# Optimization experiments

Measured on AMD Instinct MI355X. Metric: run time of the kernel, lower is better.

## Reference

```python
import jax, jax.numpy as jnp
import numpy as np

H = 128  # rnn_size

def setup_inputs() -> dict:
    key = jax.random.key(0)
    ks = jax.random.split(key, 12)
    B, T, F = 64, 2048, 64
    s = lambda k, shape, fan: jax.random.normal(k, shape, jnp.float32) * (1.0 / np.sqrt(fan))
    return {
        "x":  jax.random.normal(ks[0], (B, T, F), jnp.float32),
        # LSTM params (Keras gate order: i, f, c(g), o)
        "W":  s(ks[1], (F, 4 * H), F),
        "U":  s(ks[2], (H, 4 * H), H),
        "b":  jnp.zeros((4 * H,), jnp.float32),
        # Dense stack
        "W1": s(ks[3], (H, 128), H),   "b1": jnp.zeros((128,), jnp.float32),
        "W2": s(ks[4], (128, 128), 128), "b2": jnp.zeros((128,), jnp.float32),
        "W3": s(ks[5], (128, 32), 128),  "b3": jnp.zeros((32,), jnp.float32),
        "W4": s(ks[6], (32, 1), 32),     "b4": jnp.zeros((1,), jnp.float32),
    }

def _lstm(x, W, U, b):
    # x: [B,T,F] -> outputs h_t for all t: [B,T,H]
    B, T, _ = x.shape
    xp = jnp.einsum('btf,fg->btg', x, W) + b        # precompute input projection [B,T,4H]
    xp = jnp.transpose(xp, (1, 0, 2))               # [T,B,4H] for scan

    def step(carry, xt):
        h, c = carry
        z = xt + h @ U                              # [B,4H]
        i, f, g, o = jnp.split(z, 4, axis=-1)       # Keras gate order i,f,c,o
        i = jax.nn.sigmoid(i)
        f = jax.nn.sigmoid(f)
        g = jnp.tanh(g)
        o = jax.nn.sigmoid(o)
        c = f * c + i * g
        h = o * jnp.tanh(c)
        return (h, c), h

    h0 = jnp.zeros((B, H), x.dtype)
    c0 = jnp.zeros((B, H), x.dtype)
    _, hs = jax.lax.scan(step, (h0, c0), xp)        # hs: [T,B,H]
    return jnp.transpose(hs, (1, 0, 2))             # [B,T,H]

def reference(x, W, U, b, W1, b1, W2, b2, W3, b3, W4, b4):
    h = _lstm(x, W, U, b)                           # [B,T,H]
    h = h @ W1 + b1                                 # d1 (linear)
    h = jax.nn.relu(h @ W2 + b2)                    # d2
    h = jax.nn.relu(h @ W3 + b3)                    # d3
    out = jax.nn.sigmoid(h @ W4 + b4)               # d4 -> [B,T,1]
    return out.reshape(out.shape[0], -1, 1)         # Reshape((-1,1)) is identity here
```

## Files before the change

kernel.cpp:

```cpp
#include <hip/hip_runtime.h>
#include <hip/hip_fp16.h>
#include <cstdint>
#include <cstddef>

typedef _Float16 hh2   __attribute__((ext_vector_type(2)));
typedef _Float16 f16x8 __attribute__((ext_vector_type(8)));
typedef float    f32x4 __attribute__((ext_vector_type(4)));
typedef int      i32x4 __attribute__((ext_vector_type(4)));

__device__ __forceinline__ float fdot2u(unsigned a, unsigned b, float c) {
#if __has_builtin(__builtin_amdgcn_fdot2)
    return __builtin_amdgcn_fdot2(__builtin_bit_cast(hh2, a),
                                  __builtin_bit_cast(hh2, b), c, false);
#else
    float r;
    asm("v_dot2_f32_f16 %0, %1, %2, %3" : "=v"(r) : "v"(a), "v"(b), "v"(c));
    return r;
#endif
}

__device__ __forceinline__ unsigned packh2f(float x, float y) {
    hh2 v; v.x = (_Float16)x; v.y = (_Float16)y;
    return __builtin_bit_cast(unsigned, v);
}

__device__ __forceinline__ float ex2(float x) {
#if __has_builtin(__builtin_amdgcn_exp2f)
    return __builtin_amdgcn_exp2f(x);
#else
    return exp2f(x);
#endif
}
__device__ __forceinline__ float sig2(float x) {
    return __builtin_amdgcn_rcpf(1.f + ex2(x * -1.442695041f));
}
__device__ __forceinline__ float tanh2(float x) {
    return fmaf(2.f, __builtin_amdgcn_rcpf(1.f + ex2(x * -2.885390082f)), -1.f);
}
__device__ __forceinline__ float sigmoidf_fast(float x) {
    return __builtin_amdgcn_rcpf(1.f + __expf(-x));
}
__device__ __forceinline__ float tanhf_fast(float x) {
    float e = __expf(-2.f * fmaxf(x, -30.f));
    return (1.f - e) * __builtin_amdgcn_rcpf(1.f + e);
}

#define BAR_LGKM() asm volatile("s_waitcnt lgkmcnt(0)\n\ts_barrier" ::: "memory")

__global__ __launch_bounds__(512, 2)
void k_xprojT(const float* __restrict__ x, const float* __restrict__ W,
              const float* __restrict__ bias, __half* __restrict__ xpT,
              int B, int T)
{
    __shared__ unsigned short xst[2][16 * 64];

    const int tid = threadIdx.x;
    const int w   = tid >> 6;
    const int l   = tid & 63;
    const int lj  = l & 15;
    const int hi  = l >> 4;
    const int bb  = blockIdx.x >> 2;
    const int q   = blockIdx.x & 3;

    f16x8 Wf[4][2];
    float bc[4];
#pragma unroll
    for (int cg = 0; cg < 4; ++cg) {
        const int col = cg * 128 + w * 16 + lj;
#pragma unroll
        for (int kk = 0; kk < 2; ++kk)
#pragma unroll
            for (int j = 0; j < 8; ++j)
                Wf[cg][kk][j] = (_Float16)W[(size_t)(kk*32 + hi*8 + j) * 512 + col];
        bc[cg] = bias[col];
    }

    const int nch = (T / 4) / 16;
    const size_t rowbase = (size_t)bb * T + (size_t)q * (T / 4);

    const int srow = tid >> 5;
    const int scp  = tid & 31;

    float2 xn = *(const float2*)(x + (rowbase + srow) * 64 + scp * 2);

    for (int ch = 0; ch < nch; ++ch) {
        unsigned pk = packh2f(xn.x, xn.y);
        *(unsigned*)((char*)xst[ch & 1] +
            (((srow * 128 + scp * 4)) ^ ((srow & 7) << 4))) = pk;
        if (ch + 1 < nch)
            xn = *(const float2*)(x + (rowbase + (ch+1)*16 + srow) * 64 + scp * 2);
        BAR_LGKM();

        f16x8 Axf[2];
#pragma unroll
        for (int kk = 0; kk < 2; ++kk)
            Axf[kk] = *(const f16x8*)((char*)xst[ch & 1] +
                ((lj * 128 + kk * 64 + hi * 16) ^ ((lj & 7) << 4)));

        const size_t c8base = (rowbase + (size_t)ch * 16) >> 3;
#pragma unroll
        for (int cg = 0; cg < 4; ++cg) {
            f32x4 C = {bc[cg], bc[cg], bc[cg], bc[cg]};
            C = __builtin_amdgcn_mfma_f32_16x16x32_f16(Axf[0], Wf[cg][0], C, 0, 0, 0);
            C = __builtin_amdgcn_mfma_f32_16x16x32_f16(Axf[1], Wf[cg][1], C, 0, 0, 0);
            const int col = cg * 128 + w * 16 + lj;
            uint2 u;
            u.x = packh2f(C[0], C[1]);
            u.y = packh2f(C[2], C[3]);
            const size_t hidx = ((c8base + (hi >> 1)) * 512 + col) * 8 + (hi & 1) * 4;
            *(uint2*)((unsigned short*)xpT + hidx) = u;
        }
        BAR_LGKM();
    }
}

__global__ __launch_bounds__(512, 2)
void k_lstm7(const float* __restrict__ U, const __half* __restrict__ xpT,
             __half* __restrict__ hs, int T)
{
    __shared__ unsigned char hring[16][128];

    const int tid = threadIdx.x;
    const int w   = tid >> 6;
    const int l   = tid & 63;
    const int lj  = l & 15;
    const int hi  = l >> 4;
    const int bb  = blockIdx.x;

    i32x4 Bq[4][2];
    float dq[4];
#pragma unroll
    for (int g = 0; g < 4; ++g) {
        const int col = g * 128 + w * 16 + lj;
        float m = 0.f;
        for (int k2 = 0; k2 < 128; ++k2)
            m = fmaxf(m, fabsf(U[(size_t)k2 * 512 + col]));
        const float s = (m > 0.f) ? 127.f / m : 0.f;
        dq[g] = m * (1.f / (127.f * 127.f));
#pragma unroll
        for (int kk = 0; kk < 2; ++kk) {
            int wds[4];
#pragma unroll
            for (int d = 0; d < 4; ++d) {
                unsigned word = 0;
#pragma unroll
                for (int b = 0; b < 4; ++b) {
                    int qv = (int)rintf(
                        U[(size_t)(kk*64 + hi*16 + d*4 + b) * 512 + col] * s);
                    word |= (unsigned)(qv & 255) << (8 * b);
                }
                wds[d] = (int)word;
            }
            Bq[g][kk] = (i32x4){wds[0], wds[1], wds[2], wds[3]};
        }
    }

    if (tid < 32) ((unsigned*)hring[15])[tid] = 0u;

    const uint4* __restrict__ xb = (const uint4*)xpT;
    const size_t xrow = (size_t)bb * (T / 8) * 512;
    int colg[4];
#pragma unroll
    for (int g = 0; g < 4; ++g) colg[g] = g * 128 + w * 16 + lj;

    uint4 qA[4], qB[4];
#pragma unroll
    for (int g = 0; g < 4; ++g) {
        qA[g] = xb[xrow + 0 * 512 + colg[g]];
        qB[g] = xb[xrow + 1 * 512 + colg[g]];
    }

    __half* __restrict__ hsb = hs + (size_t)bb * T * 128;
    float cst = 0.f;

    if (((w >> 2) ^ w) & 1) __builtin_amdgcn_s_setprio(1);

    i32x4 Cq[4] = {{0,0,0,0},{0,0,0,0},{0,0,0,0},{0,0,0,0}};

    __syncthreads();

    const int nbody = T / 16;
    for (int k = 0; k < nbody; ++k) {
#pragma unroll
        for (int p = 0; p < 16; ++p) {
            if (p == 8) {
#pragma unroll
                for (int g = 0; g < 4; ++g)
                    qA[g] = xb[xrow + (size_t)(2*k + 2) * 512 + colg[g]];
            }

            const unsigned char* hrow = &hring[(p + 15) & 15][0];
            i32x4 Aq0 = *(const i32x4*)(hrow + hi * 16);
            i32x4 Aq1 = *(const i32x4*)(hrow + 64 + hi * 16);

            Cq[0][0] = 0; Cq[1][0] = 0; Cq[2][0] = 0; Cq[3][0] = 0;
#pragma unroll
            for (int g = 0; g < 4; ++g) {
                Cq[g] = __builtin_amdgcn_mfma_i32_16x16x64_i8(Aq0, Bq[g][0], Cq[g], 0, 0, 0);
                Cq[g] = __builtin_amdgcn_mfma_i32_16x16x64_i8(Aq1, Bq[g][1], Cq[g], 0, 0, 0);
            }

            float zf[4];
#pragma unroll
            for (int g = 0; g < 4; ++g) {
                const uint4 qq = (p < 8) ? qA[g] : qB[g];
                const int wsel = (p & 7) >> 1;
                unsigned uw = (wsel == 0) ? qq.x : (wsel == 1) ? qq.y
                            : (wsel == 2) ? qq.z : qq.w;
                __half2 hh = __builtin_bit_cast(__half2, uw);
                float xpf = __half2float((p & 1) ? __high2half(hh) : __low2half(hh));
                zf[g] = fmaf((float)Cq[g][0], dq[g], xpf);
            }

            float iv = sig2(zf[0]);
            float fv = sig2(zf[1]);
            float gv = tanh2(zf[2]);
            float ov = sig2(zf[3]);
            cst = fmaf(fv, cst, iv * gv);
            float h = ov * tanh2(cst);

            if (l < 16) {
                hsb[(size_t)(k * 16 + p) * 128 + w * 16 + lj] = __float2half(h);
                hring[p][w * 16 + lj] =
                    (unsigned char)(int)rintf(h * 127.f);
            }

            if (p == 15) {
#pragma unroll
                for (int g = 0; g < 4; ++g)
                    qB[g] = xb[xrow + (size_t)(2*k + 3) * 512 + colg[g]];
            }
            BAR_LGKM();
        }
    }
}

__global__ __launch_bounds__(512, 2)
void k_head(const __half* __restrict__ hs,
            const float* __restrict__ W1, const float* __restrict__ b1,
            const float* __restrict__ W2, const float* __restrict__ b2,
            const float* __restrict__ W3, const float* __restrict__ b3,
            const float* __restrict__ W4, const float* __restrict__ b4,
            float* __restrict__ out, int T)
{
    __shared__ unsigned short hstage[16 * 128];
    __shared__ unsigned short d1buf[16 * 128];
    __shared__ unsigned short d2buf[16 * 128];
    __shared__ unsigned short d3buf[16 * 40];

    const int tid = threadIdx.x;
    const int w   = tid >> 6;
    const int l   = tid & 63;
    const int lj  = l & 15;
    const int hi  = l >> 4;
    const int bb  = blockIdx.x >> 5;
    const int ch0 = (blockIdx.x & 31) * 4;

    const int col1 = w * 16 + lj;
    const int col3 = (w & 1) * 16 + lj;

    f16x8 W1f[4], W2f[4], W3f[4];
#pragma unroll
    for (int kk = 0; kk < 4; ++kk)
#pragma unroll
        for (int j = 0; j < 8; ++j) {
            W1f[kk][j] = (_Float16)W1[(size_t)(kk*32 + hi*8 + j) * 128 + col1];
            W2f[kk][j] = (_Float16)W2[(size_t)(kk*32 + hi*8 + j) * 128 + col1];
            W3f[kk][j] = (_Float16)W3[(size_t)(kk*32 + hi*8 + j) * 32 + col3];
        }
    const float b1c = b1[col1];
    const float b2c = b2[col1];
    const float b3c = b3[col3];
    unsigned w4p[16];
#pragma unroll
    for (int k2 = 0; k2 < 16; ++k2)
        w4p[k2] = packh2f(W4[2*k2], W4[2*k2 + 1]);
    const float b4v = b4[0];

    const __half* __restrict__ hsb = hs + (size_t)bb * T * 128;
    const int srow = tid >> 5;
    const int scp  = tid & 31;

    for (int ch = ch0; ch < ch0 + 4; ++ch) {
        const int t0 = ch * 16;
        uint2 hv = *(const uint2*)(hsb + (size_t)(t0 + srow) * 128 + scp * 4);
        *(uint2*)((char*)hstage + ((srow * 256 + scp * 8) ^ ((srow & 7) << 4))) = hv;
        __syncthreads();

        f16x8 A[4];
#pragma unroll
        for (int kk = 0; kk < 4; ++kk)
            A[kk] = *(const f16x8*)((char*)hstage +
                ((lj * 256 + kk * 64 + hi * 16) ^ ((lj & 7) << 4)));
        f32x4 C1 = {b1c, b1c, b1c, b1c};
#pragma unroll
        for (int kk = 0; kk < 4; ++kk)
            C1 = __builtin_amdgcn_mfma_f32_16x16x32_f16(A[kk], W1f[kk], C1, 0, 0, 0);
#pragma unroll
        for (int r = 0; r < 4; ++r) {
            const int row = hi * 4 + r;
            *(unsigned short*)((char*)d1buf + ((row * 256 + col1 * 2) ^ ((row & 7) << 4))) =
                __half_as_ushort(__float2half(C1[r]));
        }
        __syncthreads();

#pragma unroll
        for (int kk = 0; kk < 4; ++kk)
            A[kk] = *(const f16x8*)((char*)d1buf +
                ((lj * 256 + kk * 64 + hi * 16) ^ ((lj & 7) << 4)));
        f32x4 C2 = {b2c, b2c, b2c, b2c};
#pragma unroll
        for (int kk = 0; kk < 4; ++kk)
            C2 = __builtin_amdgcn_mfma_f32_16x16x32_f16(A[kk], W2f[kk], C2, 0, 0, 0);
#pragma unroll
        for (int r = 0; r < 4; ++r) {
            const int row = hi * 4 + r;
            *(unsigned short*)((char*)d2buf + ((row * 256 + col1 * 2) ^ ((row & 7) << 4))) =
                __half_as_ushort(__float2half(fmaxf(C2[r], 0.f)));
        }
        __syncthreads();

#pragma unroll
        for (int kk = 0; kk < 4; ++kk)
            A[kk] = *(const f16x8*)((char*)d2buf +
                ((lj * 256 + kk * 64 + hi * 16) ^ ((lj & 7) << 4)));
        f32x4 C3 = {b3c, b3c, b3c, b3c};
#pragma unroll
        for (int kk = 0; kk < 4; ++kk)
            C3 = __builtin_amdgcn_mfma_f32_16x16x32_f16(A[kk], W3f[kk], C3, 0, 0, 0);
        if (w < 2) {
#pragma unroll
            for (int r = 0; r < 4; ++r) {
                const int row = hi * 4 + r;
                d3buf[row * 40 + col3] =
                    __half_as_ushort(__float2half(fmaxf(C3[r], 0.f)));
            }
        }
        __syncthreads();

        if (w == 0 && l < 16) {
            const unsigned short* dr = &d3buf[l * 40];
            float s0 = b4v, s1 = 0.f;
#pragma unroll
            for (int qq = 0; qq < 4; ++qq) {
                uint4 v = *(const uint4*)(dr + qq * 8);
                s0 = fdot2u(v.x, w4p[qq*4 + 0], s0);
                s1 = fdot2u(v.y, w4p[qq*4 + 1], s1);
                s0 = fdot2u(v.z, w4p[qq*4 + 2], s0);
                s1 = fdot2u(v.w, w4p[qq*4 + 3], s1);
            }
            out[(size_t)bb * T + t0 + l] = sigmoidf_fast(s0 + s1);
        }
        __syncthreads();
    }
}

__global__ __launch_bounds__(512)
void k_lstm_fused(const float* __restrict__ U, const float* __restrict__ x,
                  const float* __restrict__ W, const float* __restrict__ bias,
                  __half* __restrict__ hs, int T)
{
    __shared__ __align__(16) unsigned hbuf[64];
    __shared__ float act[512];
    __shared__ __align__(16) unsigned xrow[32];

    const int g    = threadIdx.x;
    const int bb   = blockIdx.x;
    const int j    = g & 127;
    const int gate = g >> 7;

    unsigned ucol[64];
#pragma unroll
    for (int k2 = 0; k2 < 64; ++k2)
        ucol[k2] = packh2f(U[(2*k2)*512 + g], U[(2*k2+1)*512 + g]);
    unsigned wcol[32];
#pragma unroll
    for (int k2 = 0; k2 < 32; ++k2)
        wcol[k2] = packh2f(W[(2*k2)*512 + g], W[(2*k2+1)*512 + g]);
    const float bg = bias[g];
    const float2* __restrict__ xb2 = (const float2*)(x + (size_t)bb * T * 64);
    if (g < 32) { float2 x0 = xb2[g]; xrow[g] = packh2f(x0.x, x0.y); }
    if (g < 64) hbuf[g] = 0u;
    float c = 0.f;
    __half* __restrict__ hsb = hs + (size_t)bb * T * 128;
    __syncthreads();

    for (int t = 0; t < T; ++t) {
        float2 xn = make_float2(0.f, 0.f);
        if (g < 32 && t + 1 < T) xn = xb2[(size_t)(t + 1) * 32 + g];
        float a0 = bg, a1 = 0.f, a2 = 0.f, a3 = 0.f;
        const uint4* hr = (const uint4*)hbuf;
#pragma unroll
        for (int k8 = 0; k8 < 16; ++k8) {
            uint4 v = hr[k8];
            a0 = fdot2u(v.x, ucol[4*k8+0], a0);
            a1 = fdot2u(v.y, ucol[4*k8+1], a1);
            a2 = fdot2u(v.z, ucol[4*k8+2], a2);
            a3 = fdot2u(v.w, ucol[4*k8+3], a3);
        }
        const uint4* xr = (const uint4*)xrow;
#pragma unroll
        for (int k8 = 0; k8 < 8; ++k8) {
            uint4 v = xr[k8];
            a0 = fdot2u(v.x, wcol[4*k8+0], a0);
            a1 = fdot2u(v.y, wcol[4*k8+1], a1);
            a2 = fdot2u(v.z, wcol[4*k8+2], a2);
            a3 = fdot2u(v.w, wcol[4*k8+3], a3);
        }
        float z = (a0 + a1) + (a2 + a3);
        float a = (gate == 2) ? tanhf_fast(z) : sigmoidf_fast(z);
        act[g] = a;
        __syncthreads();
        float iv = act[j], fv = act[j + 128], gv = act[j + 256], ov = act[j + 384];
        c = fmaf(fv, c, iv * gv);
        float h = ov * tanhf_fast(c);
        if (gate == 0) {
            ((unsigned short*)hbuf)[j] = __half_as_ushort(__float2half(h));
            hsb[(size_t)t * 128 + j] = __float2half(h);
        }
        if (g < 32 && t + 1 < T) xrow[g] = packh2f(xn.x, xn.y);
        __syncthreads();
    }
}

template<bool RELU>
__global__ __launch_bounds__(512)
void k_fc128(const __half* __restrict__ in16, const float* __restrict__ Wg,
             const float* __restrict__ bias, __half* __restrict__ out16, int rows)
{
    __shared__ __align__(16) unsigned rowbuf[4 * 64];
    const int tid = threadIdx.x;
    const int n   = tid & 127;
    const int rs  = tid >> 7;
    unsigned wcol[64];
#pragma unroll
    for (int k2 = 0; k2 < 64; ++k2)
        wcol[k2] = packh2f(Wg[(2*k2)*128 + n], Wg[(2*k2+1)*128 + n]);
    const float bn = bias[n];
    for (int row0 = blockIdx.x * 4; row0 < rows; row0 += gridDim.x * 4) {
        if (tid < 256)
            rowbuf[tid] = ((const unsigned*)(in16 + (size_t)row0 * 128))[tid];
        __syncthreads();
        float a0 = bn, a1 = 0.f, a2 = 0.f, a3 = 0.f;
        const uint4* hr = (const uint4*)(rowbuf + rs * 64);
#pragma unroll
        for (int k8 = 0; k8 < 16; ++k8) {
            uint4 v = hr[k8];
            a0 = fdot2u(v.x, wcol[4*k8+0], a0);
            a1 = fdot2u(v.y, wcol[4*k8+1], a1);
            a2 = fdot2u(v.z, wcol[4*k8+2], a2);
            a3 = fdot2u(v.w, wcol[4*k8+3], a3);
        }
        float a = (a0 + a1) + (a2 + a3);
        if (RELU) a = fmaxf(a, 0.f);
        out16[(size_t)(row0 + rs) * 128 + n] = __float2half(a);
        __syncthreads();
    }
}

__global__ __launch_bounds__(512)
void k_l34(const __half* __restrict__ in16, const float* __restrict__ W3,
           const float* __restrict__ b3, const float* __restrict__ W4,
           const float* __restrict__ b4, float* __restrict__ out, int rows)
{
    __shared__ __align__(16) unsigned rowbuf[16 * 64];
    __shared__ __align__(16) unsigned short d3s[16 * 32];
    const int tid = threadIdx.x;
    const int n   = tid & 31;
    const int rs  = tid >> 5;
    unsigned w3col[64];
#pragma unroll
    for (int k2 = 0; k2 < 64; ++k2)
        w3col[k2] = packh2f(W3[(2*k2)*32 + n], W3[(2*k2+1)*32 + n]);
    unsigned w4p[16];
#pragma unroll
    for (int k2 = 0; k2 < 16; ++k2)
        w4p[k2] = packh2f(W4[2*k2], W4[2*k2+1]);
    const float b3n = b3[n], b4v = b4[0];
    for (int row0 = blockIdx.x * 16; row0 < rows; row0 += gridDim.x * 16) {
        rowbuf[tid]       = ((const unsigned*)(in16 + (size_t)row0 * 128))[tid];
        rowbuf[tid + 512] = ((const unsigned*)(in16 + (size_t)row0 * 128))[tid + 512];
        __syncthreads();
        float a0 = b3n, a1 = 0.f, a2 = 0.f, a3 = 0.f;
        const uint4* hr = (const uint4*)(rowbuf + rs * 64);
#pragma unroll
        for (int k8 = 0; k8 < 16; ++k8) {
            uint4 v = hr[k8];
            a0 = fdot2u(v.x, w3col[4*k8+0], a0);
            a1 = fdot2u(v.y, w3col[4*k8+1], a1);
            a2 = fdot2u(v.z, w3col[4*k8+2], a2);
            a3 = fdot2u(v.w, w3col[4*k8+3], a3);
        }
        float a = fmaxf((a0 + a1) + (a2 + a3), 0.f);
        d3s[rs * 32 + n] = __half_as_ushort(__float2half(a));
        __syncthreads();
        if (tid < 16) {
            const uint4* dp = (const uint4*)(d3s + tid * 32);
            float s0 = b4v, s1 = 0.f;
#pragma unroll
            for (int qq = 0; qq < 4; ++qq) {
                uint4 v = dp[qq];
                s0 = fdot2u(v.x, w4p[4*qq+0], s0);
                s1 = fdot2u(v.y, w4p[4*qq+1], s1);
                s0 = fdot2u(v.z, w4p[4*qq+2], s0);
                s1 = fdot2u(v.w, w4p[4*qq+3], s1);
            }
            out[row0 + tid] = sigmoidf_fast(s0 + s1);
        }
        __syncthreads();
    }
}

extern "C" void kernel_launch(void* const* d_in, const int* in_sizes, int n_in,
                              void* d_out, int out_size, void* d_ws, size_t ws_size,
                              hipStream_t stream)
{
    const float* x  = (const float*)d_in[0];
    const float* W  = (const float*)d_in[1];
    const float* U  = (const float*)d_in[2];
    const float* b  = (const float*)d_in[3];
    const float* W1 = (const float*)d_in[4];
    const float* b1 = (const float*)d_in[5];
    const float* W2 = (const float*)d_in[6];
    const float* b2 = (const float*)d_in[7];
    const float* W3 = (const float*)d_in[8];
    const float* b3 = (const float*)d_in[9];
    const float* W4 = (const float*)d_in[10];
    const float* b4 = (const float*)d_in[11];
    float* out = (float*)d_out;

    const int T    = 2048;
    const int rows = in_sizes[0] / 64;
    const int B    = rows / T;

    char* ws = (char*)d_ws;
    const size_t xp_bytes = (size_t)rows * 512 * sizeof(__half);
    const size_t hs_bytes = (size_t)rows * 128 * sizeof(__half);

    if (ws_size >= xp_bytes + hs_bytes) {
        __half* xpT  = (__half*)ws;
        __half* hs16 = (__half*)(ws + xp_bytes);
        k_xprojT<<<B * 4, 512, 0, stream>>>(x, W, b, xpT, B, T);
        k_lstm7<<<B, 512, 0, stream>>>(U, xpT, hs16, T);
        k_head<<<B * 32, 512, 0, stream>>>(hs16, W1, b1, W2, b2, W3, b3,
                                           W4, b4, out, T);
    } else {
        __half* hs16 = (__half*)ws;
        __half* d1   = (__half*)(ws + hs_bytes);
        __half* d2   = (__half*)ws;
        k_lstm_fused<<<B, 512, 0, stream>>>(U, x, W, b, hs16, T);
        k_fc128<false><<<1024, 512, 0, stream>>>(hs16, W1, b1, d1, rows);
        k_fc128<true ><<<1024, 512, 0, stream>>>(d1,  W2, b2, d2, rows);
        k_l34<<<1024, 512, 0, stream>>>(d2, W3, b3, W4, b4, out, rows);
    }
}
```

Before: 880.1 us.

## Spread LSTM gate activations across lane groups and exchange via LDS

Each of the four 16-lane groups in a wave now computes one gate's activation (sigmoid or tanh, written as a single exp2 and reciprocal form) instead of every lane evaluating all four gates. The results are exchanged through a small shared-memory buffer so each lane can read i/f/g/o and update the cell state. The 16-slot h ring is replaced by a 2-slot double buffer, per-lane xp loads shrink from four vectors to one, and the priority tweak is dropped. This cuts transcendental and register work on the serial recurrence path, but adds an LDS store and load round-trip inside every timestep.

```diff
diff --git a/kernel.cpp b/kernel.cpp
--- a/kernel.cpp
+++ b/kernel.cpp
@@ -115,10 +115,11 @@
 }
 
 __global__ __launch_bounds__(512, 2)
-void k_lstm7(const float* __restrict__ U, const __half* __restrict__ xpT,
+void k_lstm8(const float* __restrict__ U, const __half* __restrict__ xpT,
              __half* __restrict__ hs, int T)
 {
-    __shared__ unsigned char hring[16][128];
+    __shared__ unsigned char hbuf[2][128];
+    __shared__ float exch[512];
 
     const int tid = threadIdx.x;
     const int w   = tid >> 6;
@@ -128,15 +129,15 @@
     const int bb  = blockIdx.x;
 
     i32x4 Bq[4][2];
-    float dq[4];
+    float um[4];
 #pragma unroll
     for (int g = 0; g < 4; ++g) {
         const int col = g * 128 + w * 16 + lj;
         float m = 0.f;
         for (int k2 = 0; k2 < 128; ++k2)
             m = fmaxf(m, fabsf(U[(size_t)k2 * 512 + col]));
+        um[g] = m;
         const float s = (m > 0.f) ? 127.f / m : 0.f;
-        dq[g] = m * (1.f / (127.f * 127.f));
 #pragma unroll
         for (int kk = 0; kk < 2; ++kk) {
             int wds[4];
@@ -155,25 +156,27 @@
         }
     }
 
-    if (tid < 32) ((unsigned*)hring[15])[tid] = 0u;
+    const float um_me = (hi & 2) ? ((hi & 1) ? um[3] : um[2])
+                                 : ((hi & 1) ? um[1] : um[0]);
+    const float dq_me = um_me * (1.f / (127.f * 127.f));
+    const float mlt = (hi == 2) ? -2.885390082f : -1.442695041f;
+    const float pa  = (hi == 2) ? 2.f : 1.f;
+    const float pb  = (hi == 2) ? -1.f : 0.f;
+
+    if (tid < 32) ((unsigned*)hbuf[0])[tid] = 0u;
 
     const uint4* __restrict__ xb = (const uint4*)xpT;
     const size_t xrow = (size_t)bb * (T / 8) * 512;
-    int colg[4];
-#pragma unroll
-    for (int g = 0; g < 4; ++g) colg[g] = g * 128 + w * 16 + lj;
-
-    uint4 qA[4], qB[4];
-#pragma unroll
-    for (int g = 0; g < 4; ++g) {
-        qA[g] = xb[xrow + 0 * 512 + colg[g]];
-        qB[g] = xb[xrow + 1 * 512 + colg[g]];
-    }
+    const int col_me = hi * 128 + w * 16 + lj;
+
+    uint4 qA = xb[xrow + 0 * 512 + col_me];
+    uint4 qB = xb[xrow + 1 * 512 + col_me];
 
     __half* __restrict__ hsb = hs + (size_t)bb * T * 128;
     float cst = 0.f;
 
-    if (((w >> 2) ^ w) & 1) __builtin_amdgcn_s_setprio(1);
+    float* exw = &exch[w * 64 + lj * 4 + hi];
+    const float* exr = &exch[w * 64 + lj * 4];
 
     i32x4 Cq[4] = {{0,0,0,0},{0,0,0,0},{0,0,0,0},{0,0,0,0}};
 
@@ -183,13 +186,10 @@
     for (int k = 0; k < nbody; ++k) {
 #pragma unroll
         for (int p = 0; p < 16; ++p) {
-            if (p == 8) {
-#pragma unroll
-                for (int g = 0; g < 4; ++g)
-                    qA[g] = xb[xrow + (size_t)(2*k + 2) * 512 + colg[g]];
-            }
-
-            const unsigned char* hrow = &hring[(p + 15) & 15][0];
+            if (p == 8)
+                qA = xb[xrow + (size_t)(2*k + 2) * 512 + col_me];
+
+            const unsigned char* hrow = hbuf[p & 1];
             i32x4 Aq0 = *(const i32x4*)(hrow + hi * 16);
             i32x4 Aq1 = *(const i32x4*)(hrow + 64 + hi * 16);
 
@@ -200,36 +200,35 @@
                 Cq[g] = __builtin_amdgcn_mfma_i32_16x16x64_i8(Aq1, Bq[g][1], Cq[g], 0, 0, 0);
             }
 
-            float zf[4];
-#pragma unroll
-            for (int g = 0; g < 4; ++g) {
-                const uint4 qq = (p < 8) ? qA[g] : qB[g];
-                const int wsel = (p & 7) >> 1;
-                unsigned uw = (wsel == 0) ? qq.x : (wsel == 1) ? qq.y
-                            : (wsel == 2) ? qq.z : qq.w;
-                __half2 hh = __builtin_bit_cast(__half2, uw);
-                float xpf = __half2float((p & 1) ? __high2half(hh) : __low2half(hh));
-                zf[g] = fmaf((float)Cq[g][0], dq[g], xpf);
+            int zi = (hi & 2) ? ((hi & 1) ? Cq[3][0] : Cq[2][0])
+                              : ((hi & 1) ? Cq[1][0] : Cq[0][0]);
+
+            const uint4 qq = (p < 8) ? qA : qB;
+            const int wsel = (p & 7) >> 1;
+            unsigned uw = (wsel == 0) ? qq.x : (wsel == 1) ? qq.y
+                        : (wsel == 2) ? qq.z : qq.w;
+            __half2 hh = __builtin_bit_cast(__half2, uw);
+            float xpf = __half2float((p & 1) ? __high2half(hh) : __low2half(hh));
+
+            float zf = fmaf((float)zi, dq_me, xpf);
+
+            float e = ex2(zf * mlt);
+            float a = fmaf(pa, __builtin_amdgcn_rcpf(1.f + e), pb);
+
+            *exw = a;
+            f32x4 v = *(const f32x4*)exr;
+
+            cst = fmaf(v[1], cst, v[0] * v[2]);
+            float h = v[3] * tanh2(cst);
+
+            if (l < 16) {
+                hbuf[(p & 1) ^ 1][w * 16 + lj] =
+                    (unsigned char)(int)rintf(h * 127.f);
+                hsb[(size_t)(k * 16 + p) * 128 + w * 16 + lj] = __float2half(h);
             }
 
-            float iv = sig2(zf[0]);
-            float fv = sig2(zf[1]);
-            float gv = tanh2(zf[2]);
-            float ov = sig2(zf[3]);
-            cst = fmaf(fv, cst, iv * gv);
-            float h = ov * tanh2(cst);
-
-            if (l < 16) {
-                hsb[(size_t)(k * 16 + p) * 128 + w * 16 + lj] = __float2half(h);
-                hring[p][w * 16 + lj] =
-                    (unsigned char)(int)rintf(h * 127.f);
-            }
-
-            if (p == 15) {
-#pragma unroll
-                for (int g = 0; g < 4; ++g)
-                    qB[g] = xb[xrow + (size_t)(2*k + 3) * 512 + colg[g]];
-            }
+            if (p == 15)
+                qB = xb[xrow + (size_t)(2*k + 3) * 512 + col_me];
             BAR_LGKM();
         }
     }
@@ -541,7 +540,7 @@
         __half* xpT  = (__half*)ws;
         __half* hs16 = (__half*)(ws + xp_bytes);
         k_xprojT<<<B * 4, 512, 0, stream>>>(x, W, b, xpT, B, T);
-        k_lstm7<<<B, 512, 0, stream>>>(U, xpT, hs16, T);
+        k_lstm8<<<B, 512, 0, stream>>>(U, xpT, hs16, T);
         k_head<<<B * 32, 512, 0, stream>>>(hs16, W1, b1, W2, b2, W3, b3,
                                            W4, b4, out, T);
     } else {
```

New measurement: 792.7 us. 9.9% less time.
